# Kernel tuning notes

Hardware: AMD Instinct MI355X
Metric: run time of the kernel (lower is better)

## Reference

```python
import jax, jax.numpy as jnp
import numpy as np

D_MODEL = 1024
H = 16
D_K = D_MODEL // H  # 64


def setup_inputs() -> dict:
    key = jax.random.key(0)
    ks = jax.random.split(key, 10)
    s = 1.0 / np.sqrt(D_MODEL)
    x = jax.random.normal(ks[0], (4, 2048, D_MODEL), dtype=jnp.float32)
    # Per-head linear weights stacked: [H, d_model, d_k]
    Wq = jax.random.uniform(ks[1], (H, D_MODEL, D_K), jnp.float32, -s, s)
    bq = jax.random.uniform(ks[2], (H, D_K), jnp.float32, -s, s)
    Wk = jax.random.uniform(ks[3], (H, D_MODEL, D_K), jnp.float32, -s, s)
    bk = jax.random.uniform(ks[4], (H, D_K), jnp.float32, -s, s)
    Wv = jax.random.uniform(ks[5], (H, D_MODEL, D_K), jnp.float32, -s, s)
    bv = jax.random.uniform(ks[6], (H, D_K), jnp.float32, -s, s)
    so = 1.0 / np.sqrt(H * D_K)
    Wo = jax.random.uniform(ks[7], (H * D_K, D_MODEL), jnp.float32, -so, so)
    bo = jax.random.uniform(ks[8], (D_MODEL,), jnp.float32, -so, so)
    return {"x": x, "Wq": Wq, "bq": bq, "Wk": Wk, "bk": bk, "Wv": Wv, "bv": bv, "Wo": Wo, "bo": bo}


def reference(x, Wq, bq, Wk, bk, Wv, bv, Wo, bo):
    # x: [B, S, D]; Wq/Wk/Wv: [H, D, d_k]; b*: [H, d_k]
    q = jnp.einsum('bsd,hdk->bhsk', x, Wq) + bq[None, :, None, :]
    k = jnp.einsum('bsd,hdk->bhsk', x, Wk) + bk[None, :, None, :]
    v = jnp.einsum('bsd,hdk->bhsk', x, Wv) + bv[None, :, None, :]
    scores = jnp.einsum('bhqk,bhsk->bhqs', q, k) / np.sqrt(D_K)
    S = x.shape[1]
    causal = jnp.triu(jnp.ones((S, S), dtype=bool), k=1)  # True above diagonal
    scores = jnp.where(causal, -jnp.inf, scores)
    attn = jax.nn.softmax(scores, axis=-1)
    ctx = jnp.einsum('bhqs,bhsk->bhqk', attn, v)  # [B, H, S, d_k]
    B = x.shape[0]
    # concat heads: torch cats head outputs along last dim -> [B, S, H*d_k]
    ctx = jnp.transpose(ctx, (0, 2, 1, 3)).reshape(B, S, H * D_K)
    return ctx @ Wo + bo
```

## Files before the change

### kernel.cpp

```cpp
#include <hip/hip_runtime.h>
#include <hip/hip_bf16.h>

typedef unsigned short u16;
typedef __attribute__((ext_vector_type(8))) short short8;
typedef __attribute__((ext_vector_type(4))) short short4v;
typedef __attribute__((ext_vector_type(4))) float floatx4;

#define D_MODEL 1024
#define NH 16
#define SEQ 2048
#define BATCH 4
#define M_ROWS 8192
#define N_QKV 3072
#define PS_LD 72

#define QSCALE 0.18033688011112042f
#define EXP2_OFF 11.541560327111707f

__device__ __forceinline__ u16 f2u(float f) {
    __hip_bfloat16 h = __float2bfloat16(f);
    u16 u; __builtin_memcpy(&u, &h, 2); return u;
}

__device__ __forceinline__ void async_copy16(const u16* g, u16* l) {
    __builtin_amdgcn_global_load_lds(
        (const __attribute__((address_space(1))) unsigned int*)(g),
        (__attribute__((address_space(3))) unsigned int*)(l),
        16, 0, 0);
}

__global__ __launch_bounds__(256) void prep(
    const float* __restrict__ x,
    const float* __restrict__ Wq, const float* __restrict__ Wk,
    const float* __restrict__ Wv, const float* __restrict__ Wo,
    const float* __restrict__ bq, const float* __restrict__ bk,
    const float* __restrict__ bv, const float* __restrict__ bo,
    u16* __restrict__ xb, u16* __restrict__ Wpt, u16* __restrict__ Wot,
    float* __restrict__ biasp)
{
    __shared__ u16 T[64 * 72];
    const int tid = threadIdx.x;
    const int blk = blockIdx.x;

    if (blk < 4096) {
        size_t i = ((size_t)blk * 256 + tid) * 8;
        float4 f0 = *(const float4*)&x[i];
        float4 f1 = *(const float4*)&x[i + 4];
        u16 t[8] = {f2u(f0.x), f2u(f0.y), f2u(f0.z), f2u(f0.w),
                    f2u(f1.x), f2u(f1.y), f2u(f1.z), f2u(f1.w)};
        *(short8*)&xb[i] = *(short8*)t;
        return;
    }
    if (blk == 5120) {
        #pragma unroll
        for (int j = 0; j < 16; j++) {
            int idx = j * 256 + tid;
            float v;
            if (idx < 1024)      v = bq[idx] * QSCALE;
            else if (idx < 2048) v = bk[idx - 1024];
            else if (idx < 3072) v = bv[idx - 2048];
            else                 v = bo[idx - 3072];
            biasp[idx] = v;
        }
        return;
    }
    const int wb = blk - 4096;
    const int r = tid >> 2, s4 = (tid & 3) * 16;
    if (wb < 768) {
        int sel = wb / 256, rem = wb % 256;
        int h = rem >> 4, ktile = rem & 15;
        const float* W = (sel == 0) ? Wq : ((sel == 1) ? Wk : Wv);
        const float scale = (sel == 0) ? QSCALE : 1.0f;
        const float* src = W + ((size_t)h * 1024 + ktile * 64 + r) * 64 + s4;
        #pragma unroll
        for (int i = 0; i < 16; i++) T[(s4 + i) * 72 + r] = f2u(src[i] * scale);
        __syncthreads();
        u16 tmp[16];
        #pragma unroll
        for (int i = 0; i < 16; i++) tmp[i] = T[r * 72 + s4 + i];
        u16* dst = Wpt + ((size_t)sel * 1024 + h * 64 + r) * 1024 + ktile * 64 + s4;
        *(short8*)&dst[0] = *(short8*)&tmp[0];
        *(short8*)&dst[8] = *(short8*)&tmp[8];
    } else {
        int rem = wb - 768;
        int nt = rem >> 4, kt2 = rem & 15;
        const float* src = Wo + ((size_t)kt2 * 64 + r) * 1024 + nt * 64 + s4;
        #pragma unroll
        for (int i = 0; i < 16; i++) T[(s4 + i) * 72 + r] = f2u(src[i]);
        __syncthreads();
        u16 tmp[16];
        #pragma unroll
        for (int i = 0; i < 16; i++) tmp[i] = T[r * 72 + s4 + i];
        u16* dst = Wot + ((size_t)nt * 64 + r) * 1024 + kt2 * 64 + s4;
        *(short8*)&dst[0] = *(short8*)&tmp[0];
        *(short8*)&dst[8] = *(short8*)&tmp[8];
    }
}

__global__ __launch_bounds__(256) void vtrans(const u16* __restrict__ QKV,
                                              u16* __restrict__ Vtg) {
    __shared__ u16 T[64 * 72];
    const int bh = blockIdx.x, kt = blockIdx.y;
    const int b = bh >> 4, h = bh & 15;
    const int tid = threadIdx.x;
    const int r = tid >> 2, s4 = (tid & 3) * 16;
    const u16* vp = QKV + (size_t)(b * SEQ + kt * 64 + r) * N_QKV + 2 * D_MODEL + h * 64 + s4;
    *(short8*)&T[r * 72 + s4]     = *(const short8*)&vp[0];
    *(short8*)&T[r * 72 + s4 + 8] = *(const short8*)&vp[8];
    __syncthreads();
    u16 tmp[16];
    #pragma unroll
    for (int i = 0; i < 16; i++) tmp[i] = T[(s4 + i) * 72 + r];
    u16* op = Vtg + ((size_t)bh * 64 + r) * SEQ + kt * 64 + s4;
    *(short8*)&op[0] = *(short8*)&tmp[0];
    *(short8*)&op[8] = *(short8*)&tmp[8];
}

template <typename OT>
__global__ __launch_bounds__(256) void gemm128(
    const u16* __restrict__ A, const u16* __restrict__ Bt,
    const float* __restrict__ bias, OT* __restrict__ C,
    int M, int N, int K)
{
    __shared__ u16 As[128 * 64];
    __shared__ u16 Bs[128 * 64];
    const int tid = threadIdx.x;
    const int w = tid >> 6, lane = tid & 63;
    const int l16 = lane & 15, quad = lane >> 4;
    const int bn = blockIdx.x * 128, bm = blockIdx.y * 128;
    const int wr = (w >> 1) * 64, wc = (w & 1) * 64;

    floatx4 acc[4][4];
    #pragma unroll
    for (int i = 0; i < 4; i++)
        #pragma unroll
        for (int j = 0; j < 4; j++) acc[i][j] = (floatx4){0.f, 0.f, 0.f, 0.f};

    for (int k0 = 0; k0 < K; k0 += 64) {
        #pragma unroll
        for (int c = 0; c < 4; c++) {
            const int off = (w * 4 + c) * 1024 + lane * 16;
            const int row = off >> 7, seg = (off >> 4) & 7;
            async_copy16(A  + (size_t)(bm + row) * K + k0 + seg * 8, &As[(w * 4 + c) * 512]);
            async_copy16(Bt + (size_t)(bn + row) * K + k0 + seg * 8, &Bs[(w * 4 + c) * 512]);
        }
        __syncthreads();
        #pragma unroll
        for (int kc = 0; kc < 2; kc++) {
            short8 a[4], b[4];
            #pragma unroll
            for (int i = 0; i < 4; i++)
                a[i] = *(short8*)&As[(wr + i * 16 + l16) * 64 + kc * 32 + quad * 8];
            #pragma unroll
            for (int i = 0; i < 4; i++)
                b[i] = *(short8*)&Bs[(wc + i * 16 + l16) * 64 + kc * 32 + quad * 8];
            #pragma unroll
            for (int mm = 0; mm < 4; mm++)
                #pragma unroll
                for (int nn = 0; nn < 4; nn++)
                    acc[mm][nn] = __builtin_amdgcn_mfma_f32_16x16x32_bf16(
                        a[mm], b[nn], acc[mm][nn], 0, 0, 0);
        }
        __syncthreads();
    }

    #pragma unroll
    for (int nn = 0; nn < 4; nn++) {
        const int col = bn + wc + nn * 16 + l16;
        const float bi = bias[col];
        #pragma unroll
        for (int mm = 0; mm < 4; mm++) {
            const int row = bm + wr + mm * 16 + quad * 4;
            #pragma unroll
            for (int r = 0; r < 4; r++) {
                float v = acc[mm][nn][r] + bi;
                if constexpr (sizeof(OT) == 2) ((u16*)C)[(size_t)(row + r) * N + col] = f2u(v);
                else                           C[(size_t)(row + r) * N + col] = v;
            }
        }
    }
}

#define G256_BAR   __builtin_amdgcn_s_barrier()
#define G256_LGKM0 { asm volatile("s_waitcnt lgkmcnt(0)" ::: "memory"); \
                     __builtin_amdgcn_sched_barrier(0); }

#define G256_STG(dstbase, s0, s1) { \
    async_copy16((s0), &lds[(dstbase) + stw]); \
    async_copy16((s1), &lds[(dstbase) + 4096 + stw]); }

#define G256_STAGE_A(bb, half, kq) \
    G256_STG((bb) * 32768 + (half) * 8192, \
             pA[0] + (size_t)(half) * hstep + (kq), \
             pA[1] + (size_t)(half) * hstep + (kq))

#define G256_STAGE_B(bb, half, kq) \
    G256_STG((bb) * 32768 + 16384 + (half) * 8192, \
             pB[0] + (size_t)(half) * hstep + (kq), \
             pB[1] + (size_t)(half) * hstep + (kq))

#define G256_LDA4(dst, bb, mi0) { \
    const int _b = (bb) * 32768 + wm * 8192; \
    _Pragma("unroll") \
    for (int mi = 0; mi < 4; mi++) { \
        const int _r = _b + (((mi0) + mi) * 16 + l16) * 64; \
        dst[mi * 2]     = *(const short8*)&lds[_r + col0]; \
        dst[mi * 2 + 1] = *(const short8*)&lds[_r + col1]; \
    } }

#define G256_LDB2(dst, bb, ni0) { \
    const int _b = (bb) * 32768 + 16384 + (wn >> 1) * 8192 + (wn & 1) * 4096; \
    _Pragma("unroll") \
    for (int ni = 0; ni < 2; ni++) { \
        const int _r = _b + (((ni0) + ni) * 16 + l16) * 64; \
        dst[ni * 2]     = *(const short8*)&lds[_r + col0]; \
        dst[ni * 2 + 1] = *(const short8*)&lds[_r + col1]; \
    } }

#define G256_MMA8(av, bv, MI0, NI0) { \
    _Pragma("unroll") \
    for (int mi = 0; mi < 4; mi++) \
    _Pragma("unroll") \
    for (int ni = 0; ni < 2; ni++) { \
        acc[(MI0) + mi][(NI0) + ni] = __builtin_amdgcn_mfma_f32_16x16x32_bf16( \
            bv[ni * 2],     av[mi * 2],     acc[(MI0) + mi][(NI0) + ni], 0, 0, 0); \
        acc[(MI0) + mi][(NI0) + ni] = __builtin_amdgcn_mfma_f32_16x16x32_bf16( \
            bv[ni * 2 + 1], av[mi * 2 + 1], acc[(MI0) + mi][(NI0) + ni], 0, 0, 0); \
    } }

template <typename OT>
__global__ __launch_bounds__(512, 2) void gemm256(
    const u16* __restrict__ A, const u16* __restrict__ Bt,
    const float* __restrict__ bias, OT* __restrict__ C,
    int M, int N, int K)
{
    __shared__ u16 lds[65536];
    const int tid = threadIdx.x;
    const int w = tid >> 6, lane = tid & 63;
    const int l16 = lane & 15, quad = lane >> 4;
    const int wm = w >> 2, wn = w & 3;
    const int bn = blockIdx.x * 256, bm = blockIdx.y * 256;

    const u16* pA[2]; const u16* pB[2];
    #pragma unroll
    for (int j = 0; j < 2; j++) {
        const int d = (j * 512 + tid) * 16;
        const int s = d ^ (((d >> 7) & 7) << 4);
        const int r = s >> 7;
        const int c = (s & 127) >> 1;
        pA[j] = A  + (size_t)(bm + r) * K + c;
        pB[j] = Bt + (size_t)(bn + r) * K + c;
    }
    const size_t hstep = (size_t)128 * K;
    const int stw = w * 512;

    const int xm = (l16 & 7) << 3;
    const int col0 = (quad * 8) ^ xm;
    const int col1 = (32 + quad * 8) ^ xm;

    floatx4 acc[8][4];
    #pragma unroll
    for (int i = 0; i < 8; i++)
        #pragma unroll
        for (int j = 0; j < 4; j++) acc[i][j] = (floatx4){0.f, 0.f, 0.f, 0.f};

    G256_STAGE_A(0, 0, 0);  G256_STAGE_A(0, 1, 0);
    G256_STAGE_B(0, 0, 0);  G256_STAGE_B(0, 1, 0);
    G256_STAGE_B(1, 0, 64); G256_STAGE_B(1, 1, 64);
    asm volatile("s_waitcnt vmcnt(0)" ::: "memory");
    __syncthreads();

    short8 aL[8], aH[8], bL[4], bH[4];
    const int NKT = K >> 6;
    for (int kt = 0; kt < NKT; ++kt) {
        const int buf = kt & 1, nb = buf ^ 1;
        const int kqA = (kt + 1) << 6, kqB = (kt + 2) << 6;
        const bool stA = (kt + 1 < NKT), stB = (kt + 2 < NKT);

        G256_LDA4(aL, buf, 0);
        G256_LDB2(bL, buf, 0);
        if (stA) { G256_STAGE_A(nb, 0, kqA); }
        asm volatile("s_waitcnt lgkmcnt(8)" ::: "memory");
        G256_BAR; G256_LGKM0;
        __builtin_amdgcn_s_setprio(1); G256_MMA8(aL, bL, 0, 0);
        __builtin_amdgcn_s_setprio(0); G256_BAR;

        G256_LDB2(bH, buf, 2);
        if (stA) { G256_STAGE_A(nb, 1, kqA); }
        G256_BAR; G256_LGKM0;
        __builtin_amdgcn_s_setprio(1); G256_MMA8(aL, bH, 0, 2);
        __builtin_amdgcn_s_setprio(0); G256_BAR;

        G256_LDA4(aH, buf, 4);
        if (stB) { G256_STAGE_B(buf, 0, kqB); }
        G256_BAR; G256_LGKM0;
        __builtin_amdgcn_s_setprio(1); G256_MMA8(aH, bH, 4, 2);
        __builtin_amdgcn_s_setprio(0); G256_BAR;

        if (stB) {
            G256_STAGE_B(buf, 1, kqB);
            asm volatile("s_waitcnt vmcnt(4)" ::: "memory");
        } else if (stA) {
            asm volatile("s_waitcnt vmcnt(0)" ::: "memory");
        }
        G256_BAR;
        __builtin_amdgcn_s_setprio(1); G256_MMA8(aH, bL, 4, 0);
        __builtin_amdgcn_s_setprio(0); G256_BAR;
    }

    #pragma unroll
    for (int ni = 0; ni < 4; ni++) {
        const int col = bn + wn * 64 + ni * 16 + quad * 4;
        const float4 bi = *(const float4*)&bias[col];
        #pragma unroll
        for (int mi = 0; mi < 8; mi++) {
            const int row = bm + wm * 128 + mi * 16 + l16;
            const float v0 = acc[mi][ni][0] + bi.x;
            const float v1 = acc[mi][ni][1] + bi.y;
            const float v2 = acc[mi][ni][2] + bi.z;
            const float v3 = acc[mi][ni][3] + bi.w;
            if constexpr (sizeof(OT) == 2) {
                u16 o[4] = {f2u(v0), f2u(v1), f2u(v2), f2u(v3)};
                *(short4v*)&((u16*)C)[(size_t)row * N + col] = *(short4v*)o;
            } else {
                float4 fv = {v0, v1, v2, v3};
                *(float4*)&C[(size_t)row * N + col] = fv;
            }
        }
    }
}

__global__ __launch_bounds__(256) void attn_mfma(
    const u16* __restrict__ QKV, const u16* __restrict__ Vtg, u16* __restrict__ ctx)
{
    __shared__ u16 Ks[2][64 * 64];
    __shared__ u16 Vs[2][64 * 64];
    __shared__ u16 Ps[128 * PS_LD];

    const int bh = blockIdx.x;
    const int qt = (int)(gridDim.y - 1) - (int)blockIdx.y;
    const int b = bh >> 4, h = bh & 15;
    const int tid = threadIdx.x;
    const int w = tid >> 6, lane = tid & 63;
    const int l16 = lane & 15, quad = lane >> 4;

    const int r0 = tid >> 3,        c0 = tid & 7;
    const int r1 = (256 + tid) >> 3, c1 = tid & 7;
    const int sw0 = c0 ^ (r0 & 7), sw1 = c1 ^ (r1 & 7);

    short8 q[2][2];
    #pragma unroll
    for (int m = 0; m < 2; m++) {
        const u16* qp = QKV + (size_t)(b * SEQ + qt * 128 + w * 32 + m * 16 + l16) * N_QKV + h * 64;
        q[m][0] = *(const short8*)&qp[quad * 8];
        q[m][1] = *(const short8*)&qp[32 + quad * 8];
    }

    short8 ones8;
    #pragma unroll
    for (int i = 0; i < 8; i++) ones8[i] = (short)0x3F80;

    floatx4 O[2][4];
    floatx4 lsum[2];
    #pragma unroll
    for (int m = 0; m < 2; m++) {
        lsum[m] = (floatx4){0.f, 0.f, 0.f, 0.f};
        #pragma unroll
        for (int i = 0; i < 4; i++) O[m][i] = (floatx4){0.f, 0.f, 0.f, 0.f};
    }

    const int nkt = 2 * qt + 2;
    const int qrow_w_max = qt * 128 + w * 32 + 31;

    const size_t kbase = (size_t)(b * SEQ) * N_QKV + D_MODEL + h * 64;
    const size_t vbase = (size_t)bh * 64 * SEQ;

    const u16* kpa = QKV + kbase + (size_t)r0 * N_QKV + c0 * 8;
    const u16* kpb = QKV + kbase + (size_t)r1 * N_QKV + c1 * 8;
    const u16* vpa = Vtg + vbase + (size_t)r0 * SEQ + c0 * 8;
    const u16* vpb = Vtg + vbase + (size_t)r1 * SEQ + c1 * 8;

    {
        float4 ka = *(const float4*)kpa;
        float4 kb = *(const float4*)kpb;
        float4 va = *(const float4*)vpa;
        float4 vb = *(const float4*)vpb;
        *(float4*)&Ks[0][r0 * 64 + sw0 * 8] = ka;
        *(float4*)&Ks[0][r1 * 64 + sw1 * 8] = kb;
        *(float4*)&Vs[0][r0 * 64 + sw0 * 8] = va;
        *(float4*)&Vs[0][r1 * 64 + sw1 * 8] = vb;
    }
    kpa += (size_t)64 * N_QKV; kpb += (size_t)64 * N_QKV;
    vpa += 64; vpb += 64;
    __syncthreads();

    for (int kt = 0; kt < nkt; kt++) {
        const int buf = kt & 1;
        const bool pre = (kt + 1 < nkt);
        float4 ka, kb, va, vb;
        if (pre) {
            ka = *(const float4*)kpa;
            kb = *(const float4*)kpb;
            va = *(const float4*)vpa;
            vb = *(const float4*)vpb;
            kpa += (size_t)64 * N_QKV; kpb += (size_t)64 * N_QKV;
            vpa += 64; vpb += 64;
        }

        if (kt * 64 <= qrow_w_max) {
            short8 kf[4][2];
            #pragma unroll
            for (int ns = 0; ns < 4; ns++) {
                const int rr = ns * 16 + l16, rs = rr & 7;
                kf[ns][0] = *(short8*)&Ks[buf][rr * 64 + (quad ^ rs) * 8];
                kf[ns][1] = *(short8*)&Ks[buf][rr * 64 + ((4 + quad) ^ rs) * 8];
            }
            const bool needMask = (kt * 64 + 63 > qt * 128 + w * 32);

            #pragma unroll
            for (int m = 0; m < 2; m++) {
                floatx4 z[4];
                __builtin_amdgcn_s_setprio(1);
                #pragma unroll
                for (int ns = 0; ns < 4; ns++) {
                    floatx4 t = (floatx4){0.f, 0.f, 0.f, 0.f};
                    t = __builtin_amdgcn_mfma_f32_16x16x32_bf16(kf[ns][0], q[m][0], t, 0, 0, 0);
                    t = __builtin_amdgcn_mfma_f32_16x16x32_bf16(kf[ns][1], q[m][1], t, 0, 0, 0);
                    z[ns] = t;
                }
                __builtin_amdgcn_s_setprio(0);
                const int qrow_g = qt * 128 + w * 32 + m * 16 + l16;
                const int prow = (w * 32 + m * 16 + l16) * PS_LD;
                #pragma unroll
                for (int ns = 0; ns < 4; ns++) {
                    u16 pk[4];
                    #pragma unroll
                    for (int r = 0; r < 4; r++) {
                        float s = z[ns][r];
                        const int key = kt * 64 + ns * 16 + quad * 4 + r;
                        if (needMask && key > qrow_g) s = -INFINITY;
                        float p = __builtin_amdgcn_exp2f(s - EXP2_OFF);
                        pk[r] = f2u(p);
                    }
                    *(short4v*)&Ps[prow + ns * 16 + quad * 4] = *(short4v*)pk;
                }
            }

            short8 vf[4][2];
            #pragma unroll
            for (int ds = 0; ds < 4; ds++) {
                const int rr = ds * 16 + l16, rs = rr & 7;
                vf[ds][0] = *(short8*)&Vs[buf][rr * 64 + (quad ^ rs) * 8];
                vf[ds][1] = *(short8*)&Vs[buf][rr * 64 + ((4 + quad) ^ rs) * 8];
            }
            __builtin_amdgcn_s_setprio(1);
            #pragma unroll
            for (int m = 0; m < 2; m++) {
                const int prow = (w * 32 + m * 16 + l16) * PS_LD;
                short8 p0 = *(short8*)&Ps[prow + quad * 8];
                short8 p1 = *(short8*)&Ps[prow + 32 + quad * 8];
                lsum[m] = __builtin_amdgcn_mfma_f32_16x16x32_bf16(ones8, p0, lsum[m], 0, 0, 0);
                lsum[m] = __builtin_amdgcn_mfma_f32_16x16x32_bf16(ones8, p1, lsum[m], 0, 0, 0);
                #pragma unroll
                for (int ds = 0; ds < 4; ds++) {
                    O[m][ds] = __builtin_amdgcn_mfma_f32_16x16x32_bf16(vf[ds][0], p0, O[m][ds], 0, 0, 0);
                    O[m][ds] = __builtin_amdgcn_mfma_f32_16x16x32_bf16(vf[ds][1], p1, O[m][ds], 0, 0, 0);
                }
            }
            __builtin_amdgcn_s_setprio(0);
        }

        if (pre) {
            const int nb = buf ^ 1;
            *(float4*)&Ks[nb][r0 * 64 + sw0 * 8] = ka;
            *(float4*)&Ks[nb][r1 * 64 + sw1 * 8] = kb;
            *(float4*)&Vs[nb][r0 * 64 + sw0 * 8] = va;
            *(float4*)&Vs[nb][r1 * 64 + sw1 * 8] = vb;
        }
        __syncthreads();
    }

    #pragma unroll
    for (int m = 0; m < 2; m++) {
        const float inv = 1.0f / lsum[m][0];
        const size_t base = (size_t)(b * SEQ + qt * 128 + w * 32 + m * 16 + l16) * D_MODEL + h * 64;
        #pragma unroll
        for (int ds = 0; ds < 4; ds++) {
            u16 o[4];
            #pragma unroll
            for (int r = 0; r < 4; r++) o[r] = f2u(O[m][ds][r] * inv);
            *(short4v*)&ctx[base + ds * 16 + quad * 4] = *(short4v*)o;
        }
    }
}

extern "C" void kernel_launch(void* const* d_in, const int* in_sizes, int n_in,
                              void* d_out, int out_size, void* d_ws, size_t ws_size,
                              hipStream_t stream) {
    const float* x  = (const float*)d_in[0];
    const float* Wq = (const float*)d_in[1];
    const float* bq = (const float*)d_in[2];
    const float* Wk = (const float*)d_in[3];
    const float* bk = (const float*)d_in[4];
    const float* Wv = (const float*)d_in[5];
    const float* bv = (const float*)d_in[6];
    const float* Wo = (const float*)d_in[7];
    const float* bo = (const float*)d_in[8];
    float* out = (float*)d_out;

    char* ws = (char*)d_ws;
    float* biasp = (float*)ws;
    u16*   Wpt   = (u16*)(ws + 0x10000);
    u16*   Wot   = (u16*)(ws + 0x620000);
    u16*   xb    = (u16*)(ws + 0x840000);
    u16*   Vtg   = xb;
    u16*   QKV   = (u16*)(ws + 0x1840000);
    u16*   ctx   = (u16*)(ws + 0x4840000);

    prep<<<5121, 256, 0, stream>>>(x, Wq, Wk, Wv, Wo, bq, bk, bv, bo,
                                   xb, Wpt, Wot, biasp);

    gemm256<u16><<<dim3(N_QKV / 256, M_ROWS / 256), 512, 0, stream>>>(
        xb, Wpt, biasp, QKV, M_ROWS, N_QKV, D_MODEL);

    vtrans<<<dim3(64, 32), 256, 0, stream>>>(QKV, Vtg);

    attn_mfma<<<dim3(BATCH * NH, SEQ / 128), 256, 0, stream>>>(QKV, Vtg, ctx);

    gemm128<float><<<dim3(D_MODEL / 128, M_ROWS / 128), 256, 0, stream>>>(
        ctx, Wot, biasp + N_QKV, out, M_ROWS, D_MODEL, D_MODEL);
}
```

Baseline: 283.2 us.

## Swizzle GEMM block order and deepen A-tile prefetch in gemm256 pipeline

Remaps block indices in both GEMM kernels so that consecutive workgroups, grouped in strides of eight, share A/B tiles for better L2 reuse. In gemm256 the staging of A half-tiles is reshuffled: half of the next A tile is issued two iterations ahead, and the last MMA group now runs before the vmcnt wait and barrier, so global loads overlap more compute. The epilogue hoists the bias loads and reorders the stores row-major. The changed vmcnt counts and buffer reuse make the LDS hazards delicate, and the swizzle assumes the workgroup count is divisible by eight.

Measured after the change: 282.6 us. About the same (-0.2%).

```diff
diff --git a/kernel.cpp b/kernel.cpp
--- a/kernel.cpp
+++ b/kernel.cpp
@@ -127,7 +127,14 @@
     const int tid = threadIdx.x;
     const int w = tid >> 6, lane = tid & 63;
     const int l16 = lane & 15, quad = lane >> 4;
-    const int bn = blockIdx.x * 128, bm = blockIdx.y * 128;
+
+    const int nwgx = gridDim.x;
+    const int nwg = nwgx * gridDim.y;
+    const int lin = blockIdx.y * nwgx + blockIdx.x;
+    const int cpx = nwg >> 3;
+    const int swz = (lin & 7) * cpx + (lin >> 3);
+    const int bn = (swz % nwgx) * 128, bm = (swz / nwgx) * 128;
+
     const int wr = (w >> 1) * 64, wc = (w & 1) * 64;
 
     floatx4 acc[4][4];
@@ -239,7 +246,13 @@
     const int w = tid >> 6, lane = tid & 63;
     const int l16 = lane & 15, quad = lane >> 4;
     const int wm = w >> 2, wn = w & 3;
-    const int bn = blockIdx.x * 256, bm = blockIdx.y * 256;
+
+    const int nwgx = gridDim.x;
+    const int nwg = nwgx * gridDim.y;
+    const int lin = blockIdx.y * nwgx + blockIdx.x;
+    const int cpx = nwg >> 3;
+    const int swz = (lin & 7) * cpx + (lin >> 3);
+    const int bn = (swz % nwgx) * 256, bm = (swz / nwgx) * 256;
 
     const u16* pA[2]; const u16* pB[2];
     #pragma unroll
@@ -267,7 +280,8 @@
     G256_STAGE_A(0, 0, 0);  G256_STAGE_A(0, 1, 0);
     G256_STAGE_B(0, 0, 0);  G256_STAGE_B(0, 1, 0);
     G256_STAGE_B(1, 0, 64); G256_STAGE_B(1, 1, 64);
-    asm volatile("s_waitcnt vmcnt(0)" ::: "memory");
+    G256_STAGE_A(1, 0, 64);
+    asm volatile("s_waitcnt vmcnt(6)" ::: "memory");
     __syncthreads();
 
     short8 aL[8], aH[8], bL[4], bH[4];
@@ -275,50 +289,50 @@
     for (int kt = 0; kt < NKT; ++kt) {
         const int buf = kt & 1, nb = buf ^ 1;
         const int kqA = (kt + 1) << 6, kqB = (kt + 2) << 6;
-        const bool stA = (kt + 1 < NKT), stB = (kt + 2 < NKT);
+        const bool st1 = (kt + 1 < NKT), st2 = (kt + 2 < NKT);
 
         G256_LDA4(aL, buf, 0);
         G256_LDB2(bL, buf, 0);
-        if (stA) { G256_STAGE_A(nb, 0, kqA); }
+        if (st1) { G256_STAGE_A(nb, 1, kqA); }
         asm volatile("s_waitcnt lgkmcnt(8)" ::: "memory");
         G256_BAR; G256_LGKM0;
         __builtin_amdgcn_s_setprio(1); G256_MMA8(aL, bL, 0, 0);
         __builtin_amdgcn_s_setprio(0); G256_BAR;
 
         G256_LDB2(bH, buf, 2);
-        if (stA) { G256_STAGE_A(nb, 1, kqA); }
         G256_BAR; G256_LGKM0;
         __builtin_amdgcn_s_setprio(1); G256_MMA8(aL, bH, 0, 2);
         __builtin_amdgcn_s_setprio(0); G256_BAR;
 
         G256_LDA4(aH, buf, 4);
-        if (stB) { G256_STAGE_B(buf, 0, kqB); }
+        if (st2) { G256_STAGE_B(buf, 0, kqB); }
         G256_BAR; G256_LGKM0;
         __builtin_amdgcn_s_setprio(1); G256_MMA8(aH, bH, 4, 2);
         __builtin_amdgcn_s_setprio(0); G256_BAR;
 
-        if (stB) {
-            G256_STAGE_B(buf, 1, kqB);
-            asm volatile("s_waitcnt vmcnt(4)" ::: "memory");
-        } else if (stA) {
-            asm volatile("s_waitcnt vmcnt(0)" ::: "memory");
-        }
+        if (st2) { G256_STAGE_B(buf, 1, kqB); G256_STAGE_A(buf, 0, kqB); }
+        __builtin_amdgcn_s_setprio(1); G256_MMA8(aH, bL, 4, 0);
+        __builtin_amdgcn_s_setprio(0);
+        __builtin_amdgcn_sched_barrier(0);
+        if (st2)      { asm volatile("s_waitcnt vmcnt(6)" ::: "memory"); }
+        else if (st1) { asm volatile("s_waitcnt vmcnt(0)" ::: "memory"); }
         G256_BAR;
-        __builtin_amdgcn_s_setprio(1); G256_MMA8(aH, bL, 4, 0);
-        __builtin_amdgcn_s_setprio(0); G256_BAR;
-    }
-
-    #pragma unroll
-    for (int ni = 0; ni < 4; ni++) {
-        const int col = bn + wn * 64 + ni * 16 + quad * 4;
-        const float4 bi = *(const float4*)&bias[col];
-        #pragma unroll
-        for (int mi = 0; mi < 8; mi++) {
-            const int row = bm + wm * 128 + mi * 16 + l16;
-            const float v0 = acc[mi][ni][0] + bi.x;
-            const float v1 = acc[mi][ni][1] + bi.y;
-            const float v2 = acc[mi][ni][2] + bi.z;
-            const float v3 = acc[mi][ni][3] + bi.w;
+    }
+
+    float4 bi[4];
+    #pragma unroll
+    for (int ni = 0; ni < 4; ni++)
+        bi[ni] = *(const float4*)&bias[bn + wn * 64 + ni * 16 + quad * 4];
+    #pragma unroll
+    for (int mi = 0; mi < 8; mi++) {
+        const int row = bm + wm * 128 + mi * 16 + l16;
+        #pragma unroll
+        for (int ni = 0; ni < 4; ni++) {
+            const int col = bn + wn * 64 + ni * 16 + quad * 4;
+            const float v0 = acc[mi][ni][0] + bi[ni].x;
+            const float v1 = acc[mi][ni][1] + bi[ni].y;
+            const float v2 = acc[mi][ni][2] + bi[ni].z;
+            const float v3 = acc[mi][ni][3] + bi[ni].w;
             if constexpr (sizeof(OT) == 2) {
                 u16 o[4] = {f2u(v0), f2u(v1), f2u(v2), f2u(v3)};
                 *(short4v*)&((u16*)C)[(size_t)row * N + col] = *(short4v*)o;
```
